# Performance work log

Hardware: AMD Instinct MI355X
Metric: run time of the kernel (lower is better)

The kernel has to match this reference:

```python
import jax, jax.numpy as jnp
import numpy as np

N = 100000      # nodes
E = 1600000     # edges (avg degree 16)
F_IN = 64       # node_features_size
C1, C2 = 32, 64 # conv out channels (heads=1)
H1, NC = 128, 10


def setup_inputs() -> dict:
    key = jax.random.key(0)
    ks = jax.random.split(key, 24)
    g = lambda k, shape, s=0.1: (jax.random.normal(k, shape, jnp.float32) * s)
    inp = {
        "x": jax.random.normal(ks[0], (N, F_IN), jnp.float32),
        "edge_index": jax.random.randint(ks[1], (2, E), 0, N, jnp.int32),
        "edge_attr": jax.random.normal(ks[2], (E, 1), jnp.float32),
        # conv1 params (query/key/value/edge/skip), weights stored [in, out]
        "Wq1": g(ks[3], (F_IN, C1)), "bq1": jnp.zeros((C1,), jnp.float32),
        "Wk1": g(ks[4], (F_IN, C1)), "bk1": jnp.zeros((C1,), jnp.float32),
        "Wv1": g(ks[5], (F_IN, C1)), "bv1": jnp.zeros((C1,), jnp.float32),
        "We1": g(ks[6], (1, C1)),    "be1": jnp.zeros((C1,), jnp.float32),
        "Ws1": g(ks[7], (F_IN, C1)), "bs1": jnp.zeros((C1,), jnp.float32),
        # conv2 params
        "Wq2": g(ks[8], (C1, C2)),  "bq2": jnp.zeros((C2,), jnp.float32),
        "Wk2": g(ks[9], (C1, C2)),  "bk2": jnp.zeros((C2,), jnp.float32),
        "Wv2": g(ks[10], (C1, C2)), "bv2": jnp.zeros((C2,), jnp.float32),
        "We2": g(ks[11], (1, C2)),  "be2": jnp.zeros((C2,), jnp.float32),
        "Ws2": g(ks[12], (C1, C2)), "bs2": jnp.zeros((C2,), jnp.float32),
        # MLP head
        "W_fc1": g(ks[13], (C2, H1)), "b_fc1": jnp.zeros((H1,), jnp.float32),
        "W_fc2": g(ks[14], (H1, NC)), "b_fc2": jnp.zeros((NC,), jnp.float32),
    }
    return inp


def transformer_conv(x, src, dst, edge_attr, Wq, bq, Wk, bk, Wv, bv, We, be, Ws, bs):
    # PyG TransformerConv, heads=1, concat=True, root_weight=True, beta=False
    C = Wq.shape[1]
    q = x @ Wq + bq                       # [N, C]
    k = x @ Wk + bk                       # [N, C]
    v = x @ Wv + bv                       # [N, C]
    e = edge_attr @ We + be               # [E, C]
    ke = k[src] + e                       # [E, C]
    ve = v[src] + e                       # [E, C]
    alpha = jnp.sum(q[dst] * ke, axis=-1) / jnp.sqrt(jnp.float32(C))  # [E]
    # segment softmax over incoming edges of each target node
    m = jax.ops.segment_max(alpha, dst, num_segments=x.shape[0])
    a = jnp.exp(alpha - m[dst])
    s = jax.ops.segment_sum(a, dst, num_segments=x.shape[0])
    a = a / (s[dst] + 1e-16)
    out = jax.ops.segment_sum(a[:, None] * ve, dst, num_segments=x.shape[0])  # [N, C]
    return out + (x @ Ws + bs)            # root/skip connection


def reference(x, edge_index, edge_attr,
              Wq1, bq1, Wk1, bk1, Wv1, bv1, We1, be1, Ws1, bs1,
              Wq2, bq2, Wk2, bk2, Wv2, bv2, We2, be2, Ws2, bs2,
              W_fc1, b_fc1, W_fc2, b_fc2):
    src, dst = edge_index[0], edge_index[1]
    h = jax.nn.elu(transformer_conv(x, src, dst, edge_attr,
                                    Wq1, bq1, Wk1, bk1, Wv1, bv1, We1, be1, Ws1, bs1))
    h = jax.nn.elu(transformer_conv(h, src, dst, edge_attr,
                                    Wq2, bq2, Wk2, bk2, Wv2, bv2, We2, be2, Ws2, bs2))
    h = jax.nn.elu(h @ W_fc1 + b_fc1)
    logits = h @ W_fc2 + b_fc2
    return jax.nn.log_softmax(logits, axis=1)
```

## Files before the change

kernel.cpp:

```cpp
#include <hip/hip_runtime.h>
#include <hip/hip_fp16.h>
#include <math.h>


#define SCAN_NB 256

typedef _Float16 half8 __attribute__((ext_vector_type(8)));
typedef float f32x4 __attribute__((ext_vector_type(4)));

__global__ __launch_bounds__(256)
void count_rank_kernel(const int* __restrict__ dst, int* __restrict__ deg,
                       int* __restrict__ rank, int e) {
    for (int i = blockIdx.x * 256 + threadIdx.x; i < e; i += gridDim.x * 256)
        rank[i] = atomicAdd(deg + dst[i], 1);
}

__global__ __launch_bounds__(256)
void blocksum_kernel(const int* __restrict__ deg, int* __restrict__ bsum, int n) {
    __shared__ int ls[256];
    const int chunk = (n + gridDim.x - 1) / gridDim.x;
    const int b0 = blockIdx.x * chunk;
    const int b1 = (b0 + chunk < n) ? b0 + chunk : n;
    int s = 0;
    for (int i = b0 + threadIdx.x; i < b1; i += 256) s += deg[i];
    ls[threadIdx.x] = s;
    __syncthreads();
    for (int off = 128; off > 0; off >>= 1) {
        if (threadIdx.x < off) ls[threadIdx.x] += ls[threadIdx.x + off];
        __syncthreads();
    }
    if (threadIdx.x == 0) bsum[blockIdx.x] = ls[0];
}

__global__ __launch_bounds__(256)
void scanb_kernel(const int* __restrict__ bsum, int* __restrict__ boff,
                  int* __restrict__ total, int nb) {
    __shared__ int ls[256];
    const int t = threadIdx.x;
    int v = (t < nb) ? bsum[t] : 0;
    ls[t] = v;
    __syncthreads();
    for (int off = 1; off < 256; off <<= 1) {
        int u = (t >= off) ? ls[t - off] : 0;
        __syncthreads();
        ls[t] += u;
        __syncthreads();
    }
    if (t < nb) boff[t] = ls[t] - v;
    if (t == 255) *total = ls[255];
}

__global__ __launch_bounds__(256)
void writeptr_kernel(const int* __restrict__ deg, const int* __restrict__ boff,
                     int* __restrict__ rowptr, int n) {
    __shared__ int ls[256];
    const int chunk = (n + gridDim.x - 1) / gridDim.x;
    const int b0 = blockIdx.x * chunk;
    const int b1 = (b0 + chunk < n) ? b0 + chunk : n;
    const int tchunk = (chunk + 255) / 256;
    const int t0 = b0 + threadIdx.x * tchunk;
    const int t1 = (t0 + tchunk < b1) ? t0 + tchunk : b1;
    int s = 0;
    for (int i = t0; i < t1; ++i) s += deg[i];
    ls[threadIdx.x] = s;
    __syncthreads();
    for (int off = 1; off < 256; off <<= 1) {
        int u = (threadIdx.x >= off) ? ls[threadIdx.x - off] : 0;
        __syncthreads();
        ls[threadIdx.x] += u;
        __syncthreads();
    }
    int run = boff[blockIdx.x] + ls[threadIdx.x] - s;
    for (int i = t0; i < t1; ++i) { rowptr[i] = run; run += deg[i]; }
}

__global__ __launch_bounds__(256)
void fill_pack_kernel(const int* __restrict__ src, const int* __restrict__ dst,
                      const float* __restrict__ eattr,
                      const int* __restrict__ rowptr, const int* __restrict__ rank,
                      int2* __restrict__ ecsr, int e) {
    for (int i = blockIdx.x * 256 + threadIdx.x; i < e; i += gridDim.x * 256) {
        int p = rowptr[dst[i]] + rank[i];
        ecsr[p] = make_int2(src[i], __float_as_int(eattr[i]));
    }
}

template<int FIN, int C>
__global__ __launch_bounds__(256, 2)
void linear4_mfma_kernel(const float* __restrict__ X,
                         const float* __restrict__ Wq, const float* __restrict__ bq,
                         const float* __restrict__ Wk, const float* __restrict__ bk,
                         const float* __restrict__ Wv, const float* __restrict__ bv,
                         const float* __restrict__ Ws, const float* __restrict__ bs,
                         float* __restrict__ q, __half2* __restrict__ kv,
                         float* __restrict__ s, int n)
{
    constexpr int FOURC = 4 * C;
    constexpr int P  = FIN + 16;
    constexpr int KT = FIN / 32;
    constexpr int NT = FOURC / 16;
    __shared__ _Float16 wsh[FOURC * P] __attribute__((aligned(16)));
    __shared__ float bsh[FOURC];

    for (int i = threadIdx.x; i < FOURC * FIN; i += 256) {
        int col = i / FIN, f = i - (i / FIN) * FIN;
        float w;
        if (col < C)          w = Wq[f * C + col];
        else if (col < 2 * C) w = Ws[f * C + col - C];
        else if (col < 3 * C) w = Wk[f * C + col - 2 * C];
        else                  w = Wv[f * C + col - 3 * C];
        wsh[col * P + f] = (_Float16)w;
    }
    for (int i = threadIdx.x; i < FOURC; i += 256) {
        bsh[i] = (i < C) ? bq[i] : (i < 2 * C) ? bs[i - C]
               : (i < 3 * C) ? bk[i - 2 * C] : bv[i - 3 * C];
    }
    __syncthreads();

    const int lane = threadIdx.x & 63;
    const int wid  = threadIdx.x >> 6;
    const int m = lane & 15, g = lane >> 4;

    half8 bfrag[KT][NT];
    #pragma unroll
    for (int kt = 0; kt < KT; ++kt)
        #pragma unroll
        for (int nt = 0; nt < NT; ++nt)
            bfrag[kt][nt] = *reinterpret_cast<const half8*>(
                &wsh[(nt * 16 + m) * P + kt * 32 + g * 8]);

    const int tiles = n >> 4;
    for (int t = blockIdx.x * 4 + wid; t < tiles; t += gridDim.x * 4) {
        const int row0 = t * 16;
        const float* xr = X + (size_t)(row0 + m) * FIN + g * 8;
        half8 afrag[KT];
        #pragma unroll
        for (int kt = 0; kt < KT; ++kt) {
            float4 u = *reinterpret_cast<const float4*>(xr + kt * 32);
            float4 w = *reinterpret_cast<const float4*>(xr + kt * 32 + 4);
            afrag[kt] = half8{(_Float16)u.x, (_Float16)u.y, (_Float16)u.z, (_Float16)u.w,
                              (_Float16)w.x, (_Float16)w.y, (_Float16)w.z, (_Float16)w.w};
        }
        #pragma unroll
        for (int nt = 0; nt < 2 * C / 16; ++nt) {
            f32x4 acc = {0.f, 0.f, 0.f, 0.f};
            #pragma unroll
            for (int kt = 0; kt < KT; ++kt)
                acc = __builtin_amdgcn_mfma_f32_16x16x32_f16(afrag[kt], bfrag[kt][nt], acc, 0, 0, 0);
            const int col = nt * 16 + m;
            const float bias = bsh[col];
            float* outp = (nt < C / 16) ? q : s;
            const int cc = (nt < C / 16) ? col : col - C;
            #pragma unroll
            for (int r = 0; r < 4; ++r)
                outp[(size_t)(row0 + g * 4 + r) * C + cc] = acc[r] + bias;
        }
        #pragma unroll
        for (int t2 = 0; t2 < C / 16; ++t2) {
            const int ntK = 2 * C / 16 + t2, ntV = 3 * C / 16 + t2;
            f32x4 aK = {0.f, 0.f, 0.f, 0.f}, aV = {0.f, 0.f, 0.f, 0.f};
            #pragma unroll
            for (int kt = 0; kt < KT; ++kt) {
                aK = __builtin_amdgcn_mfma_f32_16x16x32_f16(afrag[kt], bfrag[kt][ntK], aK, 0, 0, 0);
                aV = __builtin_amdgcn_mfma_f32_16x16x32_f16(afrag[kt], bfrag[kt][ntV], aV, 0, 0, 0);
            }
            const int ck = t2 * 16 + m;
            const float bK = bsh[2 * C + ck], bV = bsh[3 * C + ck];
            #pragma unroll
            for (int r = 0; r < 4; ++r)
                kv[(size_t)(row0 + g * 4 + r) * C + ck] = __floats2half2_rn(aK[r] + bK, aV[r] + bV);
        }
    }
}

template<int FIN, int COUT>
__global__ __launch_bounds__(256, 2)
void linear_mfma_kernel(const float* __restrict__ X, const float* __restrict__ W,
                        const float* __restrict__ b, float* __restrict__ out, int n)
{
    constexpr int P  = FIN + 16;
    constexpr int KT = FIN / 32;
    constexpr int NT = COUT / 16;
    __shared__ _Float16 wsh[COUT * P] __attribute__((aligned(16)));
    __shared__ float bsh[COUT];
    for (int i = threadIdx.x; i < COUT * FIN; i += 256) {
        int col = i / FIN, f = i - (i / FIN) * FIN;
        wsh[col * P + f] = (_Float16)W[f * COUT + col];
    }
    for (int i = threadIdx.x; i < COUT; i += 256) bsh[i] = b[i];
    __syncthreads();

    const int lane = threadIdx.x & 63;
    const int wid  = threadIdx.x >> 6;
    const int m = lane & 15, g = lane >> 4;

    half8 bfrag[KT][NT];
    #pragma unroll
    for (int kt = 0; kt < KT; ++kt)
        #pragma unroll
        for (int nt = 0; nt < NT; ++nt)
            bfrag[kt][nt] = *reinterpret_cast<const half8*>(
                &wsh[(nt * 16 + m) * P + kt * 32 + g * 8]);

    const int tiles = n >> 4;
    for (int t = blockIdx.x * 4 + wid; t < tiles; t += gridDim.x * 4) {
        const int row0 = t * 16;
        const float* xr = X + (size_t)(row0 + m) * FIN + g * 8;
        half8 afrag[KT];
        #pragma unroll
        for (int kt = 0; kt < KT; ++kt) {
            float4 u = *reinterpret_cast<const float4*>(xr + kt * 32);
            float4 w = *reinterpret_cast<const float4*>(xr + kt * 32 + 4);
            afrag[kt] = half8{(_Float16)u.x, (_Float16)u.y, (_Float16)u.z, (_Float16)u.w,
                              (_Float16)w.x, (_Float16)w.y, (_Float16)w.z, (_Float16)w.w};
        }
        #pragma unroll
        for (int nt = 0; nt < NT; ++nt) {
            f32x4 acc = {0.f, 0.f, 0.f, 0.f};
            #pragma unroll
            for (int kt = 0; kt < KT; ++kt)
                acc = __builtin_amdgcn_mfma_f32_16x16x32_f16(afrag[kt], bfrag[kt][nt], acc, 0, 0, 0);
            const int col = nt * 16 + m;
            const float bias = bsh[col];
            #pragma unroll
            for (int r = 0; r < 4; ++r) {
                float hv = acc[r] + bias;
                hv = (hv > 0.f) ? hv : expm1f(hv);
                out[(size_t)(row0 + g * 4 + r) * COUT + col] = hv;
            }
        }
    }
}

template<int C>
__global__ __launch_bounds__(256)
void conv_fused_kernel(const int* __restrict__ rowptr, const int2* __restrict__ ecsr,
                       const float* __restrict__ q, const __half2* __restrict__ kv,
                       const float* __restrict__ sres,
                       const float* __restrict__ We, const float* __restrict__ be,
                       float* __restrict__ h, float scale, int n)
{
    constexpr int LPE    = C / 2;
    constexpr int EPI    = 64 / LPE;
    constexpr int LOG    = (C == 64) ? 5 : 4;
    constexpr int UNROLL = 4;
    const int wave = threadIdx.x >> 6;
    const int lane = threadIdx.x & 63;
    const int l    = lane & (LPE - 1);
    const int slot = lane >> LOG;
    const int c0   = 2 * l;
    const int node = blockIdx.x * 4 + wave;
    if (node >= n) return;

    const float2 wec = *reinterpret_cast<const float2*>(We + c0);
    const float2 bec = *reinterpret_cast<const float2*>(be + c0);
    const float2 qp  = *reinterpret_cast<const float2*>(q + (size_t)node * C + c0);
    const int r0 = rowptr[node], r1 = rowptr[node + 1];

    float ssum = 0.f, acc0 = 0.f, acc1 = 0.f;
    int j = r0 + slot;
    for (; j + (UNROLL - 1) * EPI < r1; j += UNROLL * EPI) {
        int2 epk[UNROLL]; float2 kvr[UNROLL];
        #pragma unroll
        for (int u = 0; u < UNROLL; ++u) epk[u] = ecsr[j + u * EPI];
        #pragma unroll
        for (int u = 0; u < UNROLL; ++u)
            kvr[u] = *reinterpret_cast<const float2*>(kv + (size_t)epk[u].x * C + c0);
        #pragma unroll
        for (int u = 0; u < UNROLL; ++u) {
            float ea = __int_as_float(epk[u].y);
            float e0 = fmaf(ea, wec.x, bec.x);
            float e1 = fmaf(ea, wec.y, bec.y);
            float2 f0 = __half22float2(*reinterpret_cast<__half2*>(&kvr[u].x));
            float2 f1 = __half22float2(*reinterpret_cast<__half2*>(&kvr[u].y));
            float p = fmaf(qp.x, f0.x + e0, qp.y * (f1.x + e1));
            #pragma unroll
            for (int off = LPE >> 1; off > 0; off >>= 1) p += __shfl_xor(p, off);
            float w = __expf(p * scale);
            ssum += w;
            acc0 = fmaf(w, f0.y + e0, acc0);
            acc1 = fmaf(w, f1.y + e1, acc1);
        }
    }
    for (; j < r1; j += EPI) {
        int2 epk = ecsr[j];
        float2 kvr = *reinterpret_cast<const float2*>(kv + (size_t)epk.x * C + c0);
        float ea = __int_as_float(epk.y);
        float e0 = fmaf(ea, wec.x, bec.x);
        float e1 = fmaf(ea, wec.y, bec.y);
        float2 f0 = __half22float2(*reinterpret_cast<__half2*>(&kvr.x));
        float2 f1 = __half22float2(*reinterpret_cast<__half2*>(&kvr.y));
        float p = fmaf(qp.x, f0.x + e0, qp.y * (f1.x + e1));
        #pragma unroll
        for (int off = LPE >> 1; off > 0; off >>= 1) p += __shfl_xor(p, off);
        float w = __expf(p * scale);
        ssum += w;
        acc0 = fmaf(w, f0.y + e0, acc0);
        acc1 = fmaf(w, f1.y + e1, acc1);
    }

    #pragma unroll
    for (int off = LPE; off < 64; off <<= 1) {
        ssum += __shfl_xor(ssum, off);
        acc0 += __shfl_xor(acc0, off);
        acc1 += __shfl_xor(acc1, off);
    }

    if (slot == 0) {
        float inv = 1.f / (ssum + 1e-16f);
        float2 sr = *reinterpret_cast<const float2*>(sres + (size_t)node * C + c0);
        float h0 = fmaf(acc0, inv, sr.x);
        float h1 = fmaf(acc1, inv, sr.y);
        h0 = (h0 > 0.f) ? h0 : expm1f(h0);
        h1 = (h1 > 0.f) ? h1 : expm1f(h1);
        *reinterpret_cast<float2*>(h + (size_t)node * C + c0) = make_float2(h0, h1);
    }
}

#define H1_DIM 128
#define NC_DIM 10
__global__ __launch_bounds__(256)
void head_kernel(const float* __restrict__ Hf, const float* __restrict__ W,
                 const float* __restrict__ b, float* __restrict__ out, int n)
{
    __shared__ float wsh[H1_DIM * NC_DIM];
    __shared__ float bsh[NC_DIM];
    for (int i = threadIdx.x; i < H1_DIM * NC_DIM; i += 256) wsh[i] = W[i];
    for (int i = threadIdx.x; i < NC_DIM; i += 256) bsh[i] = b[i];
    __syncthreads();
    for (int row = blockIdx.x * 256 + threadIdx.x; row < n; row += gridDim.x * 256) {
        const float* hr = Hf + (size_t)row * H1_DIM;
        float logit[NC_DIM];
        #pragma unroll
        for (int c = 0; c < NC_DIM; ++c) logit[c] = bsh[c];
        for (int f = 0; f < H1_DIM; ++f) {
            float xv = hr[f];
            #pragma unroll
            for (int c = 0; c < NC_DIM; ++c) logit[c] = fmaf(xv, wsh[f * NC_DIM + c], logit[c]);
        }
        float m = logit[0];
        #pragma unroll
        for (int c = 1; c < NC_DIM; ++c) m = fmaxf(m, logit[c]);
        float sum = 0.f;
        #pragma unroll
        for (int c = 0; c < NC_DIM; ++c) sum += __expf(logit[c] - m);
        float lse = m + logf(sum);
        #pragma unroll
        for (int c = 0; c < NC_DIM; ++c) out[(size_t)row * NC_DIM + c] = logit[c] - lse;
    }
}

extern "C" void kernel_launch(void* const* d_in, const int* in_sizes, int n_in,
                              void* d_out, int out_size, void* d_ws, size_t ws_size,
                              hipStream_t stream) {
    const float* x   = (const float*)d_in[0];
    const int*   ei  = (const int*)d_in[1];
    const float* ea  = (const float*)d_in[2];
    const float *Wq1 = (const float*)d_in[3],  *bq1 = (const float*)d_in[4];
    const float *Wk1 = (const float*)d_in[5],  *bk1 = (const float*)d_in[6];
    const float *Wv1 = (const float*)d_in[7],  *bv1 = (const float*)d_in[8];
    const float *We1 = (const float*)d_in[9],  *be1 = (const float*)d_in[10];
    const float *Ws1 = (const float*)d_in[11], *bs1 = (const float*)d_in[12];
    const float *Wq2 = (const float*)d_in[13], *bq2 = (const float*)d_in[14];
    const float *Wk2 = (const float*)d_in[15], *bk2 = (const float*)d_in[16];
    const float *Wv2 = (const float*)d_in[17], *bv2 = (const float*)d_in[18];
    const float *We2 = (const float*)d_in[19], *be2 = (const float*)d_in[20];
    const float *Ws2 = (const float*)d_in[21], *bs2 = (const float*)d_in[22];
    const float *Wf1 = (const float*)d_in[23], *bf1 = (const float*)d_in[24];
    const float *Wf2 = (const float*)d_in[25], *bf2 = (const float*)d_in[26];

    const int N = in_sizes[0] / 64;
    const int E = in_sizes[2];
    const int* src = ei;
    const int* dst = ei + E;

    float* wsf = (float*)d_ws;
    const size_t N64 = (size_t)N * 64;
    float* q      = wsf;
    __half2* kv   = (__half2*)(q + N64);
    float* s      = (float*)(kv + N64);
    float* h1     = s + N64;
    float* h2     = h1 + (size_t)N * 32;
    int* deg      = (int*)(h2 + N64);
    int* rowptr   = deg + N;
    int* bsum     = rowptr + N + 1;
    int* boff     = bsum + SCAN_NB;
    int* rank     = boff + SCAN_NB;
    int2* ecsr    = (int2*)(rank + E);
    float* hfc    = wsf;

    float* out = (float*)d_out;

    hipMemsetAsync(deg, 0, (size_t)N * 4, stream);
    count_rank_kernel<<<2048, 256, 0, stream>>>(dst, deg, rank, E);
    blocksum_kernel<<<SCAN_NB, 256, 0, stream>>>(deg, bsum, N);
    scanb_kernel<<<1, 256, 0, stream>>>(bsum, boff, rowptr + N, SCAN_NB);
    writeptr_kernel<<<SCAN_NB, 256, 0, stream>>>(deg, boff, rowptr, N);
    fill_pack_kernel<<<4096, 256, 0, stream>>>(src, dst, ea, rowptr, rank, ecsr, E);

    const int convGrid = (N + 3) / 4;

    linear4_mfma_kernel<64, 32><<<1024, 256, 0, stream>>>(
        x, Wq1, bq1, Wk1, bk1, Wv1, bv1, Ws1, bs1, q, kv, s, N);
    conv_fused_kernel<32><<<convGrid, 256, 0, stream>>>(
        rowptr, ecsr, q, kv, s, We1, be1, h1, 0.17677669529663687f, N);

    linear4_mfma_kernel<32, 64><<<1024, 256, 0, stream>>>(
        h1, Wq2, bq2, Wk2, bk2, Wv2, bv2, Ws2, bs2, q, kv, s, N);
    conv_fused_kernel<64><<<convGrid, 256, 0, stream>>>(
        rowptr, ecsr, q, kv, s, We2, be2, h2, 0.125f, N);

    linear_mfma_kernel<64, 128><<<1024, 256, 0, stream>>>(h2, Wf1, bf1, hfc, N);
    head_kernel<<<512, 256, 0, stream>>>(hfc, Wf2, bf2, out, N);
}
```

Before: 362.2 us.

## Factor edge-embedding terms out of attention loop and predicate the remainder iterations

```diff
diff --git a/kernel.cpp b/kernel.cpp
--- a/kernel.cpp
+++ b/kernel.cpp
@@ -257,60 +257,61 @@
     const float2 qp  = *reinterpret_cast<const float2*>(q + (size_t)node * C + c0);
     const int r0 = rowptr[node], r1 = rowptr[node + 1];
 
-    float ssum = 0.f, acc0 = 0.f, acc1 = 0.f;
-    int j = r0 + slot;
-    for (; j + (UNROLL - 1) * EPI < r1; j += UNROLL * EPI) {
-        int2 epk[UNROLL]; float2 kvr[UNROLL];
-        #pragma unroll
-        for (int u = 0; u < UNROLL; ++u) epk[u] = ecsr[j + u * EPI];
+    float pd1 = fmaf(qp.x, wec.x, qp.y * wec.y);
+    float pd0 = fmaf(qp.x, bec.x, qp.y * bec.y);
+    #pragma unroll
+    for (int off = LPE >> 1; off > 0; off >>= 1) {
+        pd1 += __shfl_xor(pd1, off);
+        pd0 += __shfl_xor(pd0, off);
+    }
+    const float sd1 = pd1 * scale, sd0 = pd0 * scale;
+
+    float ssum = 0.f, swea = 0.f, a0 = 0.f, a1 = 0.f;
+    const int j0 = r0 + slot;
+    const int iters = (r1 - j0 + EPI - 1) / EPI;
+    for (int it = 0; it < iters; it += UNROLL) {
+        int2 epk[UNROLL]; float2 kvr[UNROLL]; bool ok[UNROLL];
+        #pragma unroll
+        for (int u = 0; u < UNROLL; ++u) {
+            int j = j0 + (it + u) * EPI;
+            ok[u] = j < r1;
+            epk[u] = ecsr[ok[u] ? j : r0];
+        }
         #pragma unroll
         for (int u = 0; u < UNROLL; ++u)
             kvr[u] = *reinterpret_cast<const float2*>(kv + (size_t)epk[u].x * C + c0);
         #pragma unroll
         for (int u = 0; u < UNROLL; ++u) {
             float ea = __int_as_float(epk[u].y);
-            float e0 = fmaf(ea, wec.x, bec.x);
-            float e1 = fmaf(ea, wec.y, bec.y);
             float2 f0 = __half22float2(*reinterpret_cast<__half2*>(&kvr[u].x));
             float2 f1 = __half22float2(*reinterpret_cast<__half2*>(&kvr[u].y));
-            float p = fmaf(qp.x, f0.x + e0, qp.y * (f1.x + e1));
+            float p = fmaf(qp.x, f0.x, qp.y * f1.x);
             #pragma unroll
             for (int off = LPE >> 1; off > 0; off >>= 1) p += __shfl_xor(p, off);
-            float w = __expf(p * scale);
+            float w = __expf(fmaf(scale, p, fmaf(sd1, ea, sd0)));
+            w = ok[u] ? w : 0.f;
             ssum += w;
-            acc0 = fmaf(w, f0.y + e0, acc0);
-            acc1 = fmaf(w, f1.y + e1, acc1);
-        }
-    }
-    for (; j < r1; j += EPI) {
-        int2 epk = ecsr[j];
-        float2 kvr = *reinterpret_cast<const float2*>(kv + (size_t)epk.x * C + c0);
-        float ea = __int_as_float(epk.y);
-        float e0 = fmaf(ea, wec.x, bec.x);
-        float e1 = fmaf(ea, wec.y, bec.y);
-        float2 f0 = __half22float2(*reinterpret_cast<__half2*>(&kvr.x));
-        float2 f1 = __half22float2(*reinterpret_cast<__half2*>(&kvr.y));
-        float p = fmaf(qp.x, f0.x + e0, qp.y * (f1.x + e1));
-        #pragma unroll
-        for (int off = LPE >> 1; off > 0; off >>= 1) p += __shfl_xor(p, off);
-        float w = __expf(p * scale);
-        ssum += w;
-        acc0 = fmaf(w, f0.y + e0, acc0);
-        acc1 = fmaf(w, f1.y + e1, acc1);
+            swea = fmaf(w, ea, swea);
+            a0 = fmaf(w, f0.y, a0);
+            a1 = fmaf(w, f1.y, a1);
+        }
     }
 
     #pragma unroll
     for (int off = LPE; off < 64; off <<= 1) {
         ssum += __shfl_xor(ssum, off);
-        acc0 += __shfl_xor(acc0, off);
-        acc1 += __shfl_xor(acc1, off);
+        swea += __shfl_xor(swea, off);
+        a0   += __shfl_xor(a0, off);
+        a1   += __shfl_xor(a1, off);
     }
 
     if (slot == 0) {
         float inv = 1.f / (ssum + 1e-16f);
+        float t0 = fmaf(wec.x, swea, fmaf(bec.x, ssum, a0));
+        float t1 = fmaf(wec.y, swea, fmaf(bec.y, ssum, a1));
         float2 sr = *reinterpret_cast<const float2*>(sres + (size_t)node * C + c0);
-        float h0 = fmaf(acc0, inv, sr.x);
-        float h1 = fmaf(acc1, inv, sr.y);
+        float h0 = fmaf(t0, inv, sr.x);
+        float h1 = fmaf(t1, inv, sr.y);
         h0 = (h0 > 0.f) ? h0 : expm1f(h0);
         h1 = (h1 > 0.f) ? h1 : expm1f(h1);
         *reinterpret_cast<float2*>(h + (size_t)node * C + c0) = make_float2(h0, h1);
```

Result: faster. 350.7 us (-3.2%).
